# Kernel optimization log

Measured on AMD Instinct MI355X. Metric: run time of the kernel, lower is better.

The kernel has to match this reference:

```python
import jax, jax.numpy as jnp
import numpy as np

N_ENT = 100000   # n_entities
N_REL = 64       # n_relations
E_DIM = 64       # e_dim == r_dim (rel2ent is None)
K = 32           # neighbors per entity
B = 1024         # batch of seed entities
SLOPE = 0.2      # LeakyReLU negative_slope


def _xavier(key, shape, fan_in, fan_out):
    b = (6.0 / (fan_in + fan_out)) ** 0.5
    return jax.random.uniform(key, shape, jnp.float32, -b, b)


def setup_inputs() -> dict:
    key = jax.random.key(0)
    ks = jax.random.split(key, 10)
    E = _xavier(ks[0], (N_ENT, E_DIM), N_ENT, E_DIM)          # entity_embs.weight
    R = _xavier(ks[1], (N_REL, E_DIM), N_REL, E_DIM)          # relation_embs.weight
    att_w1 = _xavier(ks[2], (E_DIM, 2 * E_DIM), 2 * E_DIM, E_DIM)  # attention[0], no bias
    att_w2 = _xavier(ks[3], (E_DIM, E_DIM), E_DIM, E_DIM)          # attention[2], no bias
    att_w3 = _xavier(ks[4], (1, E_DIM), E_DIM, 1)                  # attention[4], no bias
    wx_w = _xavier(ks[5], (E_DIM, E_DIM), E_DIM, E_DIM)            # Wx[0].weight
    wx_b = jnp.zeros((E_DIM,), jnp.float32)                        # Wx[0].bias
    wc_w = _xavier(ks[6], (E_DIM, 2 * E_DIM), 2 * E_DIM, E_DIM)    # W_concat.weight
    wc_b = jnp.zeros((E_DIM,), jnp.float32)                        # W_concat.bias
    entity_idx = jax.random.randint(ks[7], (B,), 0, N_ENT)
    adj_entity = jax.random.randint(ks[8], (N_ENT, K), 0, N_ENT)
    adj_relation = jax.random.randint(ks[9], (N_ENT, K), 0, N_REL)
    return {
        "entity_idx": entity_idx, "adj_entity": adj_entity, "adj_relation": adj_relation,
        "E": E, "R": R, "att_w1": att_w1, "att_w2": att_w2, "att_w3": att_w3,
        "wx_w": wx_w, "wx_b": wx_b, "wc_w": wc_w, "wc_b": wc_b,
    }


def _lookup(W, idx):
    # nn.Embedding(max_norm=1): rows whose L2 norm exceeds 1 are renormalized.
    e = W[idx]
    n = jnp.linalg.norm(e, axis=-1, keepdims=True)
    return e * jnp.where(n > 1.0, 1.0 / (n + 1e-7), 1.0)


def _forward(entity_idx, adj_entity, adj_relation, E, R,
             att_w1, att_w2, att_w3, wx_w, wx_b, wc_w, wc_b):
    leaky = lambda x: jnp.where(x >= 0, x, SLOPE * x)
    # attention MLP on cat([h, r]): split first linear so the broadcast h term
    # is computed once per batch row instead of materializing [B, N, 2e].
    w1h, w1r = att_w1[:, :E_DIM], att_w1[:, E_DIM:]

    def gat(h, r, t):
        # h: [B, e] (broadcast over neighbors), r,t: [B, N, e]
        hid = jax.nn.relu(jnp.einsum('be,fe->bf', h, w1h)[:, None, :]
                          + jnp.einsum('bne,fe->bnf', r, w1r))
        hid = jax.nn.relu(jnp.einsum('bnf,gf->bng', hid, att_w2))
        a = jax.nn.sigmoid(jnp.einsum('bng,og->bno', hid, att_w3)[..., 0])  # [B, N]
        w = jax.nn.softmax(a, axis=-1)
        agg = jnp.einsum('bn,bne->be', w, t)       # softmax-weighted neighbor sum
        return agg @ wx_w.T + wx_b                 # per-head Linear (n_heads=1)

    Bsz = entity_idx.shape[0]
    # hop-1 / hop-2 neighbor index gathers (get_neighbors)
    ent1 = adj_entity[entity_idx]                  # [B, K]
    rel1 = adj_relation[entity_idx]                # [B, K]
    ent2 = adj_entity[ent1].reshape(Bsz, -1)       # [B, K*K]
    rel2 = adj_relation[ent1].reshape(Bsz, -1)     # [B, K*K]

    h = _lookup(E, entity_idx)                     # [B, e]
    t1 = _lookup(E, ent1)                          # [B, K, e]
    t2 = _lookup(E, ent2)                          # [B, K*K, e]
    r1 = _lookup(R, rel1)
    r2 = _lookup(R, rel2)

    # iter 0: seed entity broadcast as head
    v1 = leaky(gat(h, r1, t1))                                      # [B, e]
    emb1 = leaky(jnp.concatenate([h, v1], -1) @ wc_w.T + wc_b)      # aggregate 'concat'
    # iter 1: summed hop-1 neighborhood as head
    hsum = t1.sum(axis=1)                                           # [B, e]
    v2 = leaky(gat(hsum, r2, t2))
    emb2 = leaky(jnp.concatenate([hsum, v2], -1) @ wc_w.T + wc_b)
    # sum_aggregator 'concat': e_u = cat(embs[2], cat(embs[1], embs[0]))
    return jnp.concatenate([emb2, emb1, h], axis=-1)                # [B, 3e]


def reference(entity_idx, adj_entity, adj_relation, E, R,
              att_w1, att_w2, att_w3, wx_w, wx_b, wc_w, wc_b):
    return _forward(entity_idx, adj_entity, adj_relation, E, R,
                    att_w1, att_w2, att_w3, wx_w, wx_b, wc_w, wc_b)
```

## Files before the change

kernel.cpp:

```cpp
#include <hip/hip_runtime.h>

#define SLOPE 0.2f

__device__ __forceinline__ float leaky(float x) { return x >= 0.f ? x : SLOPE * x; }

enum : int {
  OFF_PT   = 0,
  OFF_W2T  = OFF_PT + 4096,
  OFF_A3   = OFF_W2T + 4096,
  OFF_WXT  = OFF_A3 + 64,
  OFF_WXB  = OFF_WXT + 4096,
  OFF_WCT  = OFF_WXB + 64,
  OFF_WCB  = OFF_WCT + 8192,
  OFF_W1HT = OFF_WCB + 64,
  WS_FLOATS = OFF_W1HT + 4096
};

__global__ __launch_bounds__(256) void k1_prep(
    const float* __restrict__ R, const float* __restrict__ w1,
    const float* __restrict__ w2, const float* __restrict__ w3,
    const float* __restrict__ wxw, const float* __restrict__ wxb,
    const float* __restrict__ wcw, const float* __restrict__ wcb,
    float* __restrict__ ws) {
  __shared__ float Rn[64 * 65];
  int tid = threadIdx.x, wv = tid >> 6, lane = tid & 63;
  for (int r = wv; r < 64; r += 4) {
    float v = R[r * 64 + lane];
    float ss = v * v;
    #pragma unroll
    for (int m = 1; m < 64; m <<= 1) ss += __shfl_xor(ss, m, 64);
    float n = sqrtf(ss);
    float sc = n > 1.f ? 1.f / (n + 1e-7f) : 1.f;
    Rn[r * 65 + lane] = v * sc;
  }
  __syncthreads();
  int gt = blockIdx.x * 256 + tid;
  for (int i = gt; i < 4096; i += 2048) {
    int f = i >> 6, r = i & 63;
    float acc = 0.f;
    #pragma unroll
    for (int e = 0; e < 64; ++e) acc += Rn[r * 65 + e] * w1[f * 128 + 64 + e];
    ws[OFF_PT + f * 64 + r] = acc;
  }
  for (int i = gt; i < 4096; i += 2048) {
    int f = i >> 6, g = i & 63;
    ws[OFF_W2T + i] = w2[g * 64 + f];
  }
  for (int i = gt; i < 4096; i += 2048) {
    int e = i >> 6, f = i & 63;
    ws[OFF_WXT + i]  = wxw[f * 64 + e];
    ws[OFF_W1HT + i] = w1[f * 128 + e];
  }
  for (int i = gt; i < 8192; i += 2048) {
    int e = i >> 6, f = i & 63;
    ws[OFF_WCT + i] = wcw[f * 128 + e];
  }
  if (gt < 64) {
    ws[OFF_A3 + gt]  = w3[gt];
    ws[OFF_WXB + gt] = wxb[gt];
    ws[OFF_WCB + gt] = wcb[gt];
  }
}

__global__ __launch_bounds__(256) void k_main(
    const int* __restrict__ entity_idx, const int* __restrict__ adj_entity,
    const int* __restrict__ adj_relation, const float* __restrict__ E,
    const float* __restrict__ ws, float* __restrict__ out) {
  __shared__ float s_t1[32 * 64];
  __shared__ float s_pt[64 * 64];
  __shared__ float s_partA[4][64], s_partB[4][64];
  __shared__ int   s_ent1[32], s_rel1[32];
  __shared__ int   s_ei[1024];
  __shared__ float s_w[1024];
  __shared__ float s_h[64], s_hs[64], s_hq1[64], s_hq2[64];
  __shared__ float s_at1[64], s_at2[64], s_agg1[64], s_agg2[64], s_v1[64], s_v2[64];
  __shared__ float s_L1, s_L2;
  int b = blockIdx.x, tid = threadIdx.x, wv = tid >> 6, lane = tid & 63;
  int sub = lane >> 4, eg = lane & 15;
  const float4* E4 = (const float4*)E;
  int idx = entity_idx[b];

  if (tid < 64) s_h[tid] = E[(long)idx * 64 + tid];
  if (tid >= 64 && tid < 96) {
    int i = tid - 64;
    s_ent1[i] = adj_entity[(long)idx * 32 + i];
    s_rel1[i] = adj_relation[(long)idx * 32 + i];
  }
  if (tid == 0) s_L2 = 0.f;
  for (int j = tid; j < 4096; j += 256) s_pt[j] = ws[OFF_PT + j];
  __syncthreads();

  {
    float hs = 0.f;
    #pragma unroll
    for (int k = 0; k < 8; ++k) {
      int n = wv * 8 + k;
      float v = E[(long)s_ent1[n] * 64 + lane];
      s_t1[n * 64 + lane] = v;
      hs += v;
    }
    s_partA[wv][lane] = hs;
  }
  __syncthreads();
  if (tid < 64)
    s_hs[tid] = s_partA[0][tid] + s_partA[1][tid] + s_partA[2][tid] + s_partA[3][tid];
  __syncthreads();

  {
    const float* src = (wv < 2) ? s_h : s_hs;
    int e0 = (wv & 1) * 32;
    float p = 0.f;
    #pragma unroll 8
    for (int e = 0; e < 32; ++e) p += ws[OFF_W1HT + (e0 + e) * 64 + lane] * src[e0 + e];
    s_partA[wv][lane] = p;
  }
  __syncthreads();
  if (tid < 64) s_hq1[tid] = s_partA[0][tid] + s_partA[1][tid];
  else if (tid < 128) { int i = tid - 64; s_hq2[i] = s_partA[2][i] + s_partA[3][i]; }
  __syncthreads();

  {
    int swv = __builtin_amdgcn_readfirstlane(wv);
    const float* W2T = ws + OFF_W2T;
    const float* A3  = ws + OFF_A3;
    float acc1[16], acc2[16];
    #pragma unroll
    for (int i = 0; i < 16; ++i) { acc1[i] = 0.f; acc2[i] = 0.f; }
    int g0 = swv * 16;
    #pragma unroll 2
    for (int f = 0; f < 64; ++f) {
      float ptv = s_pt[f * 64 + lane];
      float h1 = fmaxf(s_hq1[f] + ptv, 0.f);
      float h2 = fmaxf(s_hq2[f] + ptv, 0.f);
      const float* w = W2T + f * 64 + g0;
      #pragma unroll
      for (int i = 0; i < 16; ++i) { acc1[i] += w[i] * h1; acc2[i] += w[i] * h2; }
    }
    float s1 = 0.f, s2 = 0.f;
    #pragma unroll
    for (int i = 0; i < 16; ++i) {
      float a3 = A3[g0 + i];
      s1 += a3 * fmaxf(acc1[i], 0.f);
      s2 += a3 * fmaxf(acc2[i], 0.f);
    }
    s_partA[wv][lane] = s1;
    s_partB[wv][lane] = s2;
  }
  __syncthreads();
  if (tid < 64) {
    float t = s_partA[0][tid] + s_partA[1][tid] + s_partA[2][tid] + s_partA[3][tid];
    float a = 1.f / (1.f + __expf(-t));
    s_at1[tid] = __expf(a);
  } else if (tid < 128) {
    int i = tid - 64;
    float t = s_partB[0][i] + s_partB[1][i] + s_partB[2][i] + s_partB[3][i];
    float a = 1.f / (1.f + __expf(-t));
    s_at2[i] = __expf(a);
  }
  __syncthreads();

  {
    float wsum = 0.f;
    #pragma unroll
    for (int i = 0; i < 4; ++i) {
      int n = tid + i * 256;
      int j = n >> 5, i2 = n & 31;
      long base = (long)s_ent1[j] * 32 + i2;
      int ei = adj_entity[base];
      int ri = adj_relation[base];
      float wgt = s_at2[ri];
      s_ei[n] = ei;
      s_w[n] = wgt;
      wsum += wgt;
    }
    #pragma unroll
    for (int m = 1; m < 64; m <<= 1) wsum += __shfl_xor(wsum, m, 64);
    if (lane == 0) atomicAdd(&s_L2, wsum);
  }
  if (tid < 32) {
    float w = s_at1[s_rel1[tid]];
    #pragma unroll
    for (int m = 1; m < 32; m <<= 1) w += __shfl_xor(w, m, 64);
    if (tid == 0) s_L1 = w;
  }
  __syncthreads();

  {
    float4 acc = {0.f, 0.f, 0.f, 0.f};
    #pragma unroll 8
    for (int i = 0; i < 64; ++i) {
      int n = i * 16 + wv * 4 + sub;
      float wgt = s_w[n];
      float4 v = E4[(long)s_ei[n] * 16 + eg];
      acc.x += wgt * v.x; acc.y += wgt * v.y; acc.z += wgt * v.z; acc.w += wgt * v.w;
    }
    #pragma unroll
    for (int m = 16; m < 64; m <<= 1) {
      acc.x += __shfl_xor(acc.x, m, 64); acc.y += __shfl_xor(acc.y, m, 64);
      acc.z += __shfl_xor(acc.z, m, 64); acc.w += __shfl_xor(acc.w, m, 64);
    }
    if (sub == 0) {
      s_partB[wv][eg * 4 + 0] = acc.x; s_partB[wv][eg * 4 + 1] = acc.y;
      s_partB[wv][eg * 4 + 2] = acc.z; s_partB[wv][eg * 4 + 3] = acc.w;
    }
  }
  {
    float a1 = 0.f;
    #pragma unroll
    for (int k = 0; k < 8; ++k) {
      int n = wv * 8 + k;
      a1 += s_at1[s_rel1[n]] * s_t1[n * 64 + lane];
    }
    s_partA[wv][lane] = a1;
  }
  __syncthreads();
  if (tid < 64) {
    float a = s_partA[0][tid] + s_partA[1][tid] + s_partA[2][tid] + s_partA[3][tid];
    s_agg1[tid] = a / s_L1;
  } else if (tid < 128) {
    int i = tid - 64;
    float a = s_partB[0][i] + s_partB[1][i] + s_partB[2][i] + s_partB[3][i];
    s_agg2[i] = a / s_L2;
  }
  __syncthreads();

  {
    const float* src = (wv < 2) ? s_agg1 : s_agg2;
    int e0 = (wv & 1) * 32;
    float p = 0.f;
    #pragma unroll 8
    for (int e = 0; e < 32; ++e)
      p += ws[OFF_WXT + (e0 + e) * 64 + lane] * src[e0 + e];
    s_partA[wv][lane] = p;
  }
  __syncthreads();
  if (tid < 64) {
    s_v1[tid] = leaky(ws[OFF_WXB + tid] + s_partA[0][tid] + s_partA[1][tid]);
  } else if (tid < 128) {
    int i = tid - 64;
    s_v2[i] = leaky(ws[OFF_WXB + i] + s_partA[2][i] + s_partA[3][i]);
  }
  __syncthreads();

  {
    const float* src = (wv == 0) ? s_h : (wv == 1) ? s_v1 : (wv == 2) ? s_hs : s_v2;
    int e0 = (wv & 1) * 64;
    float p = 0.f;
    #pragma unroll 8
    for (int e = 0; e < 64; ++e)
      p += ws[OFF_WCT + (e0 + e) * 64 + lane] * src[e];
    s_partB[wv][lane] = p;
  }
  __syncthreads();
  if (tid < 64) {
    float o = ws[OFF_WCB + tid] + s_partB[0][tid] + s_partB[1][tid];
    out[b * 192 + 64 + tid]  = leaky(o);
    out[b * 192 + 128 + tid] = s_h[tid];
  } else if (tid < 128) {
    int i = tid - 64;
    float o = ws[OFF_WCB + i] + s_partB[2][i] + s_partB[3][i];
    out[b * 192 + i] = leaky(o);
  }
}

extern "C" void kernel_launch(void* const* d_in, const int* in_sizes, int n_in,
                              void* d_out, int out_size, void* d_ws, size_t ws_size,
                              hipStream_t stream) {
  const int* entity_idx   = (const int*)d_in[0];
  const int* adj_entity   = (const int*)d_in[1];
  const int* adj_relation = (const int*)d_in[2];
  const float* E          = (const float*)d_in[3];
  const float* R          = (const float*)d_in[4];
  const float* att_w1     = (const float*)d_in[5];
  const float* att_w2     = (const float*)d_in[6];
  const float* att_w3     = (const float*)d_in[7];
  const float* wx_w       = (const float*)d_in[8];
  const float* wx_b       = (const float*)d_in[9];
  const float* wc_w       = (const float*)d_in[10];
  const float* wc_b       = (const float*)d_in[11];
  float* out              = (float*)d_out;
  float* ws               = (float*)d_ws;

  hipLaunchKernelGGL(k1_prep, dim3(8), dim3(256), 0, stream,
                     R, att_w1, att_w2, att_w3, wx_w, wx_b, wc_w, wc_b, ws);
  hipLaunchKernelGGL(k_main, dim3(1024), dim3(256), 0, stream,
                     entity_idx, adj_entity, adj_relation, E, ws, out);
}
```

Measured before the change: 162.9 us.

## Double block size to 512 threads and split per-block work across eight waves

Raises the main kernel to 512 threads (8 waves) with launch bounds targeting higher occupancy, and re-partitions every per-entity stage (hop-1 gather, MLP projections, attention accumulations, K*K neighbor gather, output linear) across the eight waves with wider partial-sum reductions. It drops the LDS staging of the precomputed relation projection table and reads it from global/cache directly. It also batches four independent float4 gathers per iteration to raise memory-level parallelism. The cost is more reductions, more synchronisation participants, and possible register pressure under the tighter launch bound.

```diff
diff --git a/kernel.cpp b/kernel.cpp
--- a/kernel.cpp
+++ b/kernel.cpp
@@ -62,13 +62,12 @@
   }
 }
 
-__global__ __launch_bounds__(256) void k_main(
+__global__ __launch_bounds__(512, 8) void k_main(
     const int* __restrict__ entity_idx, const int* __restrict__ adj_entity,
     const int* __restrict__ adj_relation, const float* __restrict__ E,
     const float* __restrict__ ws, float* __restrict__ out) {
   __shared__ float s_t1[32 * 64];
-  __shared__ float s_pt[64 * 64];
-  __shared__ float s_partA[4][64], s_partB[4][64];
+  __shared__ float s_partA[8][64], s_partB[8][64];
   __shared__ int   s_ent1[32], s_rel1[32];
   __shared__ int   s_ei[1024];
   __shared__ float s_w[1024];
@@ -87,14 +86,13 @@
     s_rel1[i] = adj_relation[(long)idx * 32 + i];
   }
   if (tid == 0) s_L2 = 0.f;
-  for (int j = tid; j < 4096; j += 256) s_pt[j] = ws[OFF_PT + j];
   __syncthreads();
 
   {
     float hs = 0.f;
     #pragma unroll
-    for (int k = 0; k < 8; ++k) {
-      int n = wv * 8 + k;
+    for (int k = 0; k < 4; ++k) {
+      int n = wv * 4 + k;
       float v = E[(long)s_ent1[n] * 64 + lane];
       s_t1[n * 64 + lane] = v;
       hs += v;
@@ -102,43 +100,52 @@
     s_partA[wv][lane] = hs;
   }
   __syncthreads();
-  if (tid < 64)
-    s_hs[tid] = s_partA[0][tid] + s_partA[1][tid] + s_partA[2][tid] + s_partA[3][tid];
-  __syncthreads();
-
-  {
-    const float* src = (wv < 2) ? s_h : s_hs;
-    int e0 = (wv & 1) * 32;
+  if (tid < 64) {
+    float t = 0.f;
+    #pragma unroll
+    for (int w = 0; w < 8; ++w) t += s_partA[w][tid];
+    s_hs[tid] = t;
+  }
+  __syncthreads();
+
+  {
+    const float* src = (wv < 4) ? s_h : s_hs;
+    int e0 = (wv & 3) * 16;
     float p = 0.f;
-    #pragma unroll 8
-    for (int e = 0; e < 32; ++e) p += ws[OFF_W1HT + (e0 + e) * 64 + lane] * src[e0 + e];
-    s_partA[wv][lane] = p;
-  }
-  __syncthreads();
-  if (tid < 64) s_hq1[tid] = s_partA[0][tid] + s_partA[1][tid];
-  else if (tid < 128) { int i = tid - 64; s_hq2[i] = s_partA[2][i] + s_partA[3][i]; }
+    #pragma unroll
+    for (int e = 0; e < 16; ++e) p += ws[OFF_W1HT + (e0 + e) * 64 + lane] * src[e0 + e];
+    s_partB[wv][lane] = p;
+  }
+  __syncthreads();
+  if (tid < 64) {
+    s_hq1[tid] = s_partB[0][tid] + s_partB[1][tid] + s_partB[2][tid] + s_partB[3][tid];
+  } else if (tid < 128) {
+    int i = tid - 64;
+    s_hq2[i] = s_partB[4][i] + s_partB[5][i] + s_partB[6][i] + s_partB[7][i];
+  }
   __syncthreads();
 
   {
     int swv = __builtin_amdgcn_readfirstlane(wv);
     const float* W2T = ws + OFF_W2T;
     const float* A3  = ws + OFF_A3;
-    float acc1[16], acc2[16];
-    #pragma unroll
-    for (int i = 0; i < 16; ++i) { acc1[i] = 0.f; acc2[i] = 0.f; }
-    int g0 = swv * 16;
+    const float* PT  = ws + OFF_PT;
+    float acc1[8], acc2[8];
+    #pragma unroll
+    for (int i = 0; i < 8; ++i) { acc1[i] = 0.f; acc2[i] = 0.f; }
+    int g0 = swv * 8;
     #pragma unroll 2
     for (int f = 0; f < 64; ++f) {
-      float ptv = s_pt[f * 64 + lane];
+      float ptv = PT[f * 64 + lane];
       float h1 = fmaxf(s_hq1[f] + ptv, 0.f);
       float h2 = fmaxf(s_hq2[f] + ptv, 0.f);
       const float* w = W2T + f * 64 + g0;
       #pragma unroll
-      for (int i = 0; i < 16; ++i) { acc1[i] += w[i] * h1; acc2[i] += w[i] * h2; }
+      for (int i = 0; i < 8; ++i) { acc1[i] += w[i] * h1; acc2[i] += w[i] * h2; }
     }
     float s1 = 0.f, s2 = 0.f;
     #pragma unroll
-    for (int i = 0; i < 16; ++i) {
+    for (int i = 0; i < 8; ++i) {
       float a3 = A3[g0 + i];
       s1 += a3 * fmaxf(acc1[i], 0.f);
       s2 += a3 * fmaxf(acc2[i], 0.f);
@@ -148,12 +155,16 @@
   }
   __syncthreads();
   if (tid < 64) {
-    float t = s_partA[0][tid] + s_partA[1][tid] + s_partA[2][tid] + s_partA[3][tid];
+    float t = 0.f;
+    #pragma unroll
+    for (int w = 0; w < 8; ++w) t += s_partA[w][tid];
     float a = 1.f / (1.f + __expf(-t));
     s_at1[tid] = __expf(a);
   } else if (tid < 128) {
     int i = tid - 64;
-    float t = s_partB[0][i] + s_partB[1][i] + s_partB[2][i] + s_partB[3][i];
+    float t = 0.f;
+    #pragma unroll
+    for (int w = 0; w < 8; ++w) t += s_partB[w][i];
     float a = 1.f / (1.f + __expf(-t));
     s_at2[i] = __expf(a);
   }
@@ -162,8 +173,8 @@
   {
     float wsum = 0.f;
     #pragma unroll
-    for (int i = 0; i < 4; ++i) {
-      int n = tid + i * 256;
+    for (int i = 0; i < 2; ++i) {
+      int n = tid + i * 512;
       int j = n >> 5, i2 = n & 31;
       long base = (long)s_ent1[j] * 32 + i2;
       int ei = adj_entity[base];
@@ -187,12 +198,18 @@
 
   {
     float4 acc = {0.f, 0.f, 0.f, 0.f};
-    #pragma unroll 8
-    for (int i = 0; i < 64; ++i) {
-      int n = i * 16 + wv * 4 + sub;
-      float wgt = s_w[n];
-      float4 v = E4[(long)s_ei[n] * 16 + eg];
-      acc.x += wgt * v.x; acc.y += wgt * v.y; acc.z += wgt * v.z; acc.w += wgt * v.w;
+    for (int t = 0; t < 8; ++t) {
+      float4 v[4];
+      int nb = t * 4 * 32 + wv * 4 + sub;
+      #pragma unroll
+      for (int j = 0; j < 4; ++j)
+        v[j] = E4[(long)s_ei[nb + j * 32] * 16 + eg];
+      #pragma unroll
+      for (int j = 0; j < 4; ++j) {
+        float wgt = s_w[nb + j * 32];
+        acc.x += wgt * v[j].x; acc.y += wgt * v[j].y;
+        acc.z += wgt * v[j].z; acc.w += wgt * v[j].w;
+      }
     }
     #pragma unroll
     for (int m = 16; m < 64; m <<= 1) {
@@ -207,58 +224,68 @@
   {
     float a1 = 0.f;
     #pragma unroll
-    for (int k = 0; k < 8; ++k) {
-      int n = wv * 8 + k;
+    for (int k = 0; k < 4; ++k) {
+      int n = wv * 4 + k;
       a1 += s_at1[s_rel1[n]] * s_t1[n * 64 + lane];
     }
     s_partA[wv][lane] = a1;
   }
   __syncthreads();
   if (tid < 64) {
-    float a = s_partA[0][tid] + s_partA[1][tid] + s_partA[2][tid] + s_partA[3][tid];
+    float a = 0.f;
+    #pragma unroll
+    for (int w = 0; w < 8; ++w) a += s_partA[w][tid];
     s_agg1[tid] = a / s_L1;
   } else if (tid < 128) {
     int i = tid - 64;
-    float a = s_partB[0][i] + s_partB[1][i] + s_partB[2][i] + s_partB[3][i];
+    float a = 0.f;
+    #pragma unroll
+    for (int w = 0; w < 8; ++w) a += s_partB[w][i];
     s_agg2[i] = a / s_L2;
   }
   __syncthreads();
 
   {
-    const float* src = (wv < 2) ? s_agg1 : s_agg2;
-    int e0 = (wv & 1) * 32;
+    const float* src = (wv < 4) ? s_agg1 : s_agg2;
+    int e0 = (wv & 3) * 16;
+    float p = 0.f;
+    #pragma unroll
+    for (int e = 0; e < 16; ++e)
+      p += ws[OFF_WXT + (e0 + e) * 64 + lane] * src[e0 + e];
+    s_partA[wv][lane] = p;
+  }
+  __syncthreads();
+  if (tid < 64) {
+    float p = s_partA[0][tid] + s_partA[1][tid] + s_partA[2][tid] + s_partA[3][tid];
+    s_v1[tid] = leaky(ws[OFF_WXB + tid] + p);
+  } else if (tid < 128) {
+    int i = tid - 64;
+    float p = s_partA[4][i] + s_partA[5][i] + s_partA[6][i] + s_partA[7][i];
+    s_v2[i] = leaky(ws[OFF_WXB + i] + p);
+  }
+  __syncthreads();
+
+  {
+    int half = wv >> 2, q = wv & 3;
+    const float* src = (q < 2) ? (half ? s_hs : s_h) : (half ? s_v2 : s_v1);
+    int e0 = q * 32;
+    int o0 = (q & 1) * 32;
     float p = 0.f;
     #pragma unroll 8
     for (int e = 0; e < 32; ++e)
-      p += ws[OFF_WXT + (e0 + e) * 64 + lane] * src[e0 + e];
-    s_partA[wv][lane] = p;
-  }
-  __syncthreads();
-  if (tid < 64) {
-    s_v1[tid] = leaky(ws[OFF_WXB + tid] + s_partA[0][tid] + s_partA[1][tid]);
-  } else if (tid < 128) {
-    int i = tid - 64;
-    s_v2[i] = leaky(ws[OFF_WXB + i] + s_partA[2][i] + s_partA[3][i]);
-  }
-  __syncthreads();
-
-  {
-    const float* src = (wv == 0) ? s_h : (wv == 1) ? s_v1 : (wv == 2) ? s_hs : s_v2;
-    int e0 = (wv & 1) * 64;
-    float p = 0.f;
-    #pragma unroll 8
-    for (int e = 0; e < 64; ++e)
-      p += ws[OFF_WCT + (e0 + e) * 64 + lane] * src[e];
+      p += ws[OFF_WCT + (e0 + e) * 64 + lane] * src[o0 + e];
     s_partB[wv][lane] = p;
   }
   __syncthreads();
   if (tid < 64) {
-    float o = ws[OFF_WCB + tid] + s_partB[0][tid] + s_partB[1][tid];
+    float o = ws[OFF_WCB + tid] + s_partB[0][tid] + s_partB[1][tid]
+            + s_partB[2][tid] + s_partB[3][tid];
     out[b * 192 + 64 + tid]  = leaky(o);
     out[b * 192 + 128 + tid] = s_h[tid];
   } else if (tid < 128) {
     int i = tid - 64;
-    float o = ws[OFF_WCB + i] + s_partB[2][i] + s_partB[3][i];
+    float o = ws[OFF_WCB + i] + s_partB[4][i] + s_partB[5][i]
+            + s_partB[6][i] + s_partB[7][i];
     out[b * 192 + i] = leaky(o);
   }
 }
@@ -283,6 +310,6 @@
 
   hipLaunchKernelGGL(k1_prep, dim3(8), dim3(256), 0, stream,
                      R, att_w1, att_w2, att_w3, wx_w, wx_b, wc_w, wc_b, ws);
-  hipLaunchKernelGGL(k_main, dim3(1024), dim3(256), 0, stream,
+  hipLaunchKernelGGL(k_main, dim3(1024), dim3(512), 0, stream,
                      entity_idx, adj_entity, adj_relation, E, ws, out);
 }
```

New measurement: 165.8 us. No clear change (+1.8%).

## Convert entity table to bf16 in prep kernel and gather bf16 for hop-2

Applied to the files above, without the earlier changes.

The prep kernel gains extra blocks that convert the full entity embedding table to packed bf16 in the workspace each call. The hop-2 weighted aggregation then gathers 16-byte bf16 rows instead of float4 fp32, halving the bytes per gathered neighbor. PT is read from global memory instead of being staged in shared memory, which reduces LDS use. The cost is a full-table conversion pass on every call and reduced precision in the hop-2 aggregation.

```diff
diff --git a/kernel.cpp b/kernel.cpp
--- a/kernel.cpp
+++ b/kernel.cpp
@@ -13,7 +13,8 @@
   OFF_WCT  = OFF_WXB + 64,
   OFF_WCB  = OFF_WCT + 8192,
   OFF_W1HT = OFF_WCB + 64,
-  WS_FLOATS = OFF_W1HT + 4096
+  WS_FLOATS = OFF_W1HT + 4096,
+  EBF_U32  = 3200000
 };
 
 __global__ __launch_bounds__(256) void k1_prep(
@@ -21,9 +22,24 @@
     const float* __restrict__ w2, const float* __restrict__ w3,
     const float* __restrict__ wxw, const float* __restrict__ wxb,
     const float* __restrict__ wcw, const float* __restrict__ wcb,
-    float* __restrict__ ws) {
+    const float* __restrict__ E, float* __restrict__ ws) {
+  int tid = threadIdx.x;
+  if (blockIdx.x >= 8) {
+    const float2* E2 = (const float2*)E;
+    unsigned* Ebf = (unsigned*)ws + WS_FLOATS;
+    int stride = (gridDim.x - 8) * 256;
+    for (int i = (blockIdx.x - 8) * 256 + tid; i < EBF_U32; i += stride) {
+      float2 f = E2[i];
+      unsigned ua = __float_as_uint(f.x);
+      ua += 0x7FFFu + ((ua >> 16) & 1u);
+      unsigned ub = __float_as_uint(f.y);
+      ub += 0x7FFFu + ((ub >> 16) & 1u);
+      Ebf[i] = (ua >> 16) | (ub & 0xFFFF0000u);
+    }
+    return;
+  }
   __shared__ float Rn[64 * 65];
-  int tid = threadIdx.x, wv = tid >> 6, lane = tid & 63;
+  int wv = tid >> 6, lane = tid & 63;
   for (int r = wv; r < 64; r += 4) {
     float v = R[r * 64 + lane];
     float ss = v * v;
@@ -67,7 +83,6 @@
     const int* __restrict__ adj_relation, const float* __restrict__ E,
     const float* __restrict__ ws, float* __restrict__ out) {
   __shared__ float s_t1[32 * 64];
-  __shared__ float s_pt[64 * 64];
   __shared__ float s_partA[4][64], s_partB[4][64];
   __shared__ int   s_ent1[32], s_rel1[32];
   __shared__ int   s_ei[1024];
@@ -76,8 +91,6 @@
   __shared__ float s_at1[64], s_at2[64], s_agg1[64], s_agg2[64], s_v1[64], s_v2[64];
   __shared__ float s_L1, s_L2;
   int b = blockIdx.x, tid = threadIdx.x, wv = tid >> 6, lane = tid & 63;
-  int sub = lane >> 4, eg = lane & 15;
-  const float4* E4 = (const float4*)E;
   int idx = entity_idx[b];
 
   if (tid < 64) s_h[tid] = E[(long)idx * 64 + tid];
@@ -87,7 +100,6 @@
     s_rel1[i] = adj_relation[(long)idx * 32 + i];
   }
   if (tid == 0) s_L2 = 0.f;
-  for (int j = tid; j < 4096; j += 256) s_pt[j] = ws[OFF_PT + j];
   __syncthreads();
 
   {
@@ -112,24 +124,25 @@
     float p = 0.f;
     #pragma unroll 8
     for (int e = 0; e < 32; ++e) p += ws[OFF_W1HT + (e0 + e) * 64 + lane] * src[e0 + e];
-    s_partA[wv][lane] = p;
-  }
-  __syncthreads();
-  if (tid < 64) s_hq1[tid] = s_partA[0][tid] + s_partA[1][tid];
-  else if (tid < 128) { int i = tid - 64; s_hq2[i] = s_partA[2][i] + s_partA[3][i]; }
+    s_partB[wv][lane] = p;
+  }
+  __syncthreads();
+  if (tid < 64) s_hq1[tid] = s_partB[0][tid] + s_partB[1][tid];
+  else if (tid < 128) { int i = tid - 64; s_hq2[i] = s_partB[2][i] + s_partB[3][i]; }
   __syncthreads();
 
   {
     int swv = __builtin_amdgcn_readfirstlane(wv);
     const float* W2T = ws + OFF_W2T;
     const float* A3  = ws + OFF_A3;
+    const float* PT  = ws + OFF_PT;
     float acc1[16], acc2[16];
     #pragma unroll
     for (int i = 0; i < 16; ++i) { acc1[i] = 0.f; acc2[i] = 0.f; }
     int g0 = swv * 16;
     #pragma unroll 2
     for (int f = 0; f < 64; ++f) {
-      float ptv = s_pt[f * 64 + lane];
+      float ptv = PT[f * 64 + lane];
       float h1 = fmaxf(s_hq1[f] + ptv, 0.f);
       float h2 = fmaxf(s_hq2[f] + ptv, 0.f);
       const float* w = W2T + f * 64 + g0;
@@ -186,22 +199,41 @@
   __syncthreads();
 
   {
-    float4 acc = {0.f, 0.f, 0.f, 0.f};
-    #pragma unroll 8
-    for (int i = 0; i < 64; ++i) {
-      int n = i * 16 + wv * 4 + sub;
-      float wgt = s_w[n];
-      float4 v = E4[(long)s_ei[n] * 16 + eg];
-      acc.x += wgt * v.x; acc.y += wgt * v.y; acc.z += wgt * v.z; acc.w += wgt * v.w;
-    }
-    #pragma unroll
-    for (int m = 16; m < 64; m <<= 1) {
-      acc.x += __shfl_xor(acc.x, m, 64); acc.y += __shfl_xor(acc.y, m, 64);
-      acc.z += __shfl_xor(acc.z, m, 64); acc.w += __shfl_xor(acc.w, m, 64);
-    }
-    if (sub == 0) {
-      s_partB[wv][eg * 4 + 0] = acc.x; s_partB[wv][eg * 4 + 1] = acc.y;
-      s_partB[wv][eg * 4 + 2] = acc.z; s_partB[wv][eg * 4 + 3] = acc.w;
+    const uint4* Ebf = (const uint4*)((const unsigned*)ws + WS_FLOATS);
+    int sub8 = lane >> 3, eg8 = lane & 7;
+    float acc[8];
+    #pragma unroll
+    for (int k = 0; k < 8; ++k) acc[k] = 0.f;
+    for (int t = 0; t < 16; ++t) {
+      uint4 v[2];
+      float wgt[2];
+      #pragma unroll
+      for (int j = 0; j < 2; ++j) {
+        int n = (t * 2 + j) * 32 + wv * 8 + sub8;
+        v[j] = Ebf[(long)s_ei[n] * 8 + eg8];
+        wgt[j] = s_w[n];
+      }
+      #pragma unroll
+      for (int j = 0; j < 2; ++j) {
+        float w = wgt[j];
+        acc[0] += w * __uint_as_float(v[j].x << 16);
+        acc[1] += w * __uint_as_float(v[j].x & 0xFFFF0000u);
+        acc[2] += w * __uint_as_float(v[j].y << 16);
+        acc[3] += w * __uint_as_float(v[j].y & 0xFFFF0000u);
+        acc[4] += w * __uint_as_float(v[j].z << 16);
+        acc[5] += w * __uint_as_float(v[j].z & 0xFFFF0000u);
+        acc[6] += w * __uint_as_float(v[j].w << 16);
+        acc[7] += w * __uint_as_float(v[j].w & 0xFFFF0000u);
+      }
+    }
+    #pragma unroll
+    for (int m = 8; m < 64; m <<= 1) {
+      #pragma unroll
+      for (int k = 0; k < 8; ++k) acc[k] += __shfl_xor(acc[k], m, 64);
+    }
+    if (sub8 == 0) {
+      #pragma unroll
+      for (int k = 0; k < 8; ++k) s_partB[wv][eg8 * 8 + k] = acc[k];
     }
   }
   {
@@ -281,8 +313,8 @@
   float* out              = (float*)d_out;
   float* ws               = (float*)d_ws;
 
-  hipLaunchKernelGGL(k1_prep, dim3(8), dim3(256), 0, stream,
-                     R, att_w1, att_w2, att_w3, wx_w, wx_b, wc_w, wc_b, ws);
+  hipLaunchKernelGGL(k1_prep, dim3(1608), dim3(256), 0, stream,
+                     R, att_w1, att_w2, att_w3, wx_w, wx_b, wc_w, wc_b, E, ws);
   hipLaunchKernelGGL(k_main, dim3(1024), dim3(256), 0, stream,
                      entity_idx, adj_entity, adj_relation, E, ws, out);
 }
```

Measured after the change: 168.0 us. 1.03x slower.

## Prefetch hop-2 adjacency early, drop shared PT staging, batch gather loads

Applied to the files above, without the earlier changes.

The hop-2 adjacency index and relation reads now run at kernel start, with each relation packed into the top byte of the entity index. This overlaps their latency with the attention MLP instead of stalling afterward. The 16KB shared-memory copy of the PT table is removed and PT is read straight from global memory, cutting LDS use and a staging pass, which may raise occupancy. The weighted gather loop issues four float4 loads before accumulating so more memory requests are in flight. Packing assumes entity IDs fit in 24 bits, which holds for 100k entities.

```diff
diff --git a/kernel.cpp b/kernel.cpp
--- a/kernel.cpp
+++ b/kernel.cpp
@@ -22,8 +22,9 @@
     const float* __restrict__ wxw, const float* __restrict__ wxb,
     const float* __restrict__ wcw, const float* __restrict__ wcb,
     float* __restrict__ ws) {
+  int tid = threadIdx.x;
   __shared__ float Rn[64 * 65];
-  int tid = threadIdx.x, wv = tid >> 6, lane = tid & 63;
+  int wv = tid >> 6, lane = tid & 63;
   for (int r = wv; r < 64; r += 4) {
     float v = R[r * 64 + lane];
     float ss = v * v;
@@ -67,17 +68,14 @@
     const int* __restrict__ adj_relation, const float* __restrict__ E,
     const float* __restrict__ ws, float* __restrict__ out) {
   __shared__ float s_t1[32 * 64];
-  __shared__ float s_pt[64 * 64];
   __shared__ float s_partA[4][64], s_partB[4][64];
   __shared__ int   s_ent1[32], s_rel1[32];
-  __shared__ int   s_ei[1024];
+  __shared__ unsigned s_ei[1024];
   __shared__ float s_w[1024];
   __shared__ float s_h[64], s_hs[64], s_hq1[64], s_hq2[64];
   __shared__ float s_at1[64], s_at2[64], s_agg1[64], s_agg2[64], s_v1[64], s_v2[64];
   __shared__ float s_L1, s_L2;
   int b = blockIdx.x, tid = threadIdx.x, wv = tid >> 6, lane = tid & 63;
-  int sub = lane >> 4, eg = lane & 15;
-  const float4* E4 = (const float4*)E;
   int idx = entity_idx[b];
 
   if (tid < 64) s_h[tid] = E[(long)idx * 64 + tid];
@@ -87,9 +85,17 @@
     s_rel1[i] = adj_relation[(long)idx * 32 + i];
   }
   if (tid == 0) s_L2 = 0.f;
-  for (int j = tid; j < 4096; j += 256) s_pt[j] = ws[OFF_PT + j];
-  __syncthreads();
-
+  __syncthreads();
+
+  #pragma unroll
+  for (int i = 0; i < 4; ++i) {
+    int n = tid + i * 256;
+    int j = n >> 5, i2 = n & 31;
+    long base = (long)s_ent1[j] * 32 + i2;
+    unsigned ei = (unsigned)adj_entity[base];
+    unsigned ri = (unsigned)adj_relation[base];
+    s_ei[n] = ei | (ri << 24);
+  }
   {
     float hs = 0.f;
     #pragma unroll
@@ -112,24 +118,25 @@
     float p = 0.f;
     #pragma unroll 8
     for (int e = 0; e < 32; ++e) p += ws[OFF_W1HT + (e0 + e) * 64 + lane] * src[e0 + e];
-    s_partA[wv][lane] = p;
-  }
-  __syncthreads();
-  if (tid < 64) s_hq1[tid] = s_partA[0][tid] + s_partA[1][tid];
-  else if (tid < 128) { int i = tid - 64; s_hq2[i] = s_partA[2][i] + s_partA[3][i]; }
+    s_partB[wv][lane] = p;
+  }
+  __syncthreads();
+  if (tid < 64) s_hq1[tid] = s_partB[0][tid] + s_partB[1][tid];
+  else if (tid < 128) { int i = tid - 64; s_hq2[i] = s_partB[2][i] + s_partB[3][i]; }
   __syncthreads();
 
   {
     int swv = __builtin_amdgcn_readfirstlane(wv);
     const float* W2T = ws + OFF_W2T;
     const float* A3  = ws + OFF_A3;
+    const float* PT  = ws + OFF_PT;
     float acc1[16], acc2[16];
     #pragma unroll
     for (int i = 0; i < 16; ++i) { acc1[i] = 0.f; acc2[i] = 0.f; }
     int g0 = swv * 16;
     #pragma unroll 2
     for (int f = 0; f < 64; ++f) {
-      float ptv = s_pt[f * 64 + lane];
+      float ptv = PT[f * 64 + lane];
       float h1 = fmaxf(s_hq1[f] + ptv, 0.f);
       float h2 = fmaxf(s_hq2[f] + ptv, 0.f);
       const float* w = W2T + f * 64 + g0;
@@ -164,12 +171,7 @@
     #pragma unroll
     for (int i = 0; i < 4; ++i) {
       int n = tid + i * 256;
-      int j = n >> 5, i2 = n & 31;
-      long base = (long)s_ent1[j] * 32 + i2;
-      int ei = adj_entity[base];
-      int ri = adj_relation[base];
-      float wgt = s_at2[ri];
-      s_ei[n] = ei;
+      float wgt = s_at2[s_ei[n] >> 24];
       s_w[n] = wgt;
       wsum += wgt;
     }
@@ -186,13 +188,25 @@
   __syncthreads();
 
   {
+    const float4* E4 = (const float4*)E;
+    int sub = lane >> 4, eg = lane & 15;
     float4 acc = {0.f, 0.f, 0.f, 0.f};
-    #pragma unroll 8
-    for (int i = 0; i < 64; ++i) {
-      int n = i * 16 + wv * 4 + sub;
-      float wgt = s_w[n];
-      float4 v = E4[(long)s_ei[n] * 16 + eg];
-      acc.x += wgt * v.x; acc.y += wgt * v.y; acc.z += wgt * v.z; acc.w += wgt * v.w;
+    #pragma unroll 1
+    for (int t = 0; t < 16; ++t) {
+      float4 v[4];
+      float wgt[4];
+      #pragma unroll
+      for (int j = 0; j < 4; ++j) {
+        int n = (t * 4 + j) * 16 + wv * 4 + sub;
+        v[j] = E4[(long)(s_ei[n] & 0xFFFFFFu) * 16 + eg];
+        wgt[j] = s_w[n];
+      }
+      #pragma unroll
+      for (int j = 0; j < 4; ++j) {
+        float w = wgt[j];
+        acc.x += w * v[j].x; acc.y += w * v[j].y;
+        acc.z += w * v[j].z; acc.w += w * v[j].w;
+      }
     }
     #pragma unroll
     for (int m = 16; m < 64; m <<= 1) {
```

After: 161.5 us. About the same (-0.8%).
